# Kernel optimization log

Hardware: AMD Instinct MI355X
Metric: run time of the kernel (lower is better)

## Reference

```python
import jax, jax.numpy as jnp
import numpy as np

SHAPES = [(100, 168), (50, 84), (25, 42)]  # per-level (h, w)
HEADS, LEVELS, POINTS, EMBED = 8, 3, 8, 256
D_ANCHORS = 4  # num_Z_anchors; POINTS % D_ANCHORS == 0


def _bilinear_sample(v_l, loc, h, w):
    # v_l: [B, H, h*w, d]; loc: [B, nq, H, P, 2] normalized sampling locations
    B, nq, H, P, _ = loc.shape
    d = v_l.shape[-1]
    # F.grid_sample(align_corners=False, padding_mode='zeros'): pixel = loc*size - 0.5
    x = loc[..., 0] * w - 0.5
    y = loc[..., 1] * h - 0.5
    x0 = jnp.floor(x)
    y0 = jnp.floor(y)
    lx = x - x0
    ly = y - y0
    x0 = x0.astype(jnp.int32)
    y0 = y0.astype(jnp.int32)

    def gather(xi, yi):
        valid = ((xi >= 0) & (xi < w) & (yi >= 0) & (yi < h)).astype(v_l.dtype)
        idx = jnp.clip(yi, 0, h - 1) * w + jnp.clip(xi, 0, w - 1)  # [B,nq,H,P]
        idx = jnp.transpose(idx, (0, 2, 1, 3)).reshape(B, H, nq * P)
        vals = jnp.take_along_axis(v_l, idx[..., None], axis=2)  # [B,H,nq*P,d]
        vals = jnp.transpose(vals.reshape(B, H, nq, P, d), (0, 2, 1, 3, 4))
        return vals * valid[..., None]

    v00 = gather(x0, y0)
    v10 = gather(x0 + 1, y0)
    v01 = gather(x0, y0 + 1)
    v11 = gather(x0 + 1, y0 + 1)
    wx, wy = lx[..., None], ly[..., None]
    return (v00 * (1 - wx) * (1 - wy) + v10 * wx * (1 - wy)
            + v01 * (1 - wx) * wy + v11 * wx * wy)


def _msda(q, v, ref, Wv, bv, Ws, b_off, Wa, ba):
    # MSDeformableAttention3D: q [B,nq,C], v [B,nv,C], ref [B,nq,D,2]
    B, nq, C = q.shape
    nv = v.shape[1]
    d = C // HEADS
    val = (v @ Wv + bv).reshape(B, nv, HEADS, d).transpose(0, 2, 1, 3)  # [B,H,nv,d]
    off = (q @ Ws + b_off).reshape(B, nq, HEADS, LEVELS, POINTS, 2)
    aw = jax.nn.softmax((q @ Wa + ba).reshape(B, nq, HEADS, LEVELS * POINTS), axis=-1)
    aw = aw.reshape(B, nq, HEADS, LEVELS, POINTS)
    norm = jnp.array([[w, h] for (h, w) in SHAPES], dtype=q.dtype)  # offset_normalizer (w,h)
    off = off / norm[None, None, None, :, None, :]
    off = off.reshape(B, nq, HEADS, LEVELS, POINTS // D_ANCHORS, D_ANCHORS, 2)
    loc = ref[:, :, None, None, None, :, :] + off  # sampling_locations
    loc = loc.reshape(B, nq, HEADS, LEVELS, POINTS, 2)
    out = jnp.zeros((B, nq, HEADS, d), q.dtype)
    start = 0
    for lvl, (h, w) in enumerate(SHAPES):
        v_l = val[:, :, start:start + h * w, :]
        start += h * w
        s = _bilinear_sample(v_l, loc[:, :, :, lvl], h, w)  # [B,nq,H,P,d]
        out = out + jnp.einsum('bqhpd,bqhp->bqhd', s, aw[:, :, :, lvl])
    return out.reshape(B, nq, C)


def _forward(query, key, value, query_pos, reference_points_cam, bev_mask,
             Wv, bv, Ws, b_off, Wa, ba, Wo, bo):
    bs, nq, C = query.shape
    ncam = key.shape[0]
    inp_residual = query
    q = query + query_pos
    # key/value: [num_cams, l, bs, C] -> [bs*num_cams, l, C]
    v = jnp.transpose(value, (2, 0, 1, 3)).reshape(bs * ncam, -1, C)
    # dense equivalent of the per-camera query rebatching: run MSDA on all
    # queries per camera, then mask out non-hit queries (identical math)
    qc = jnp.broadcast_to(q[:, None], (bs, ncam, nq, C)).reshape(bs * ncam, nq, C)
    ref = jnp.transpose(reference_points_cam, (1, 0, 2, 3, 4)).reshape(bs * ncam, nq, D_ANCHORS, 2)
    out = _msda(qc, v, ref, Wv, bv, Ws, b_off, Wa, ba).reshape(bs, ncam, nq, C)
    hit = jnp.transpose(bev_mask.sum(-1) > 0, (1, 0, 2)).astype(out.dtype)  # [bs,ncam,nq]
    slots = (out * hit[..., None]).sum(axis=1)
    count = jnp.clip(hit.sum(axis=1), 1.0, None)
    slots = slots / count[..., None]
    slots = slots @ Wo + bo
    return slots + inp_residual  # dropout is identity at inference


def setup_inputs() -> dict:
    key0 = jax.random.key(0)
    ks = jax.random.split(key0, 12)
    bs, ncam, nq = 1, 6, 4096
    nv = sum(h * w for h, w in SHAPES)
    f = jnp.float32
    s = 0.02
    inp = {}
    inp['query'] = jax.random.normal(ks[0], (bs, nq, EMBED), f)
    inp['key'] = jax.random.normal(ks[1], (ncam, nv, bs, EMBED), f)
    inp['value'] = jax.random.normal(ks[2], (ncam, nv, bs, EMBED), f)
    inp['query_pos'] = jax.random.normal(ks[3], (bs, nq, EMBED), f)
    inp['reference_points_cam'] = jax.random.uniform(ks[4], (ncam, bs, nq, D_ANCHORS, 2), f)
    inp['bev_mask'] = jax.random.bernoulli(ks[5], 0.9, (ncam, bs, nq, D_ANCHORS))
    inp['spatial_shapes'] = jnp.array(SHAPES, dtype=jnp.int32)
    inp['level_start_index'] = jnp.array(np.cumsum([0] + [h * w for h, w in SHAPES[:-1]]), dtype=jnp.int32)
    inp['Wv'] = jax.random.normal(ks[6], (EMBED, EMBED), f) * s
    inp['bv'] = jnp.zeros((EMBED,), f)
    inp['Ws'] = jax.random.normal(ks[7], (EMBED, HEADS * LEVELS * POINTS * 2), f) * s
    inp['b_off'] = jax.random.normal(ks[8], (HEADS * LEVELS * POINTS * 2,), f) * 0.5
    inp['Wa'] = jax.random.normal(ks[9], (EMBED, HEADS * LEVELS * POINTS), f) * s
    inp['ba'] = jnp.zeros((HEADS * LEVELS * POINTS,), f)
    inp['Wo'] = jax.random.normal(ks[10], (EMBED, EMBED), f) * s
    inp['bo'] = jnp.zeros((EMBED,), f)
    return inp


def reference(query, key, value, query_pos, reference_points_cam, bev_mask,
              spatial_shapes, level_start_index,
              Wv, bv, Ws, b_off, Wa, ba, Wo, bo):
    return _forward(query, key, value, query_pos, reference_points_cam, bev_mask,
                    Wv, bv, Ws, b_off, Wa, ba, Wo, bo)
```

## Files before the change

kernel.cpp:

```cpp
#include <hip/hip_runtime.h>
#include <stdint.h>

#define NQ 4096
#define NCAM 6
#define NV 22050
#define M_TOTAL (NCAM * NV)

typedef __bf16 bf16x8 __attribute__((ext_vector_type(8)));
typedef float f32x4 __attribute__((ext_vector_type(4)));
typedef unsigned int u32x4 __attribute__((ext_vector_type(4)));

__device__ __forceinline__ unsigned short f2bf(float f) {
    union { float f; uint32_t u; } v; v.f = f;
    uint32_t u = v.u;
    uint32_t r = (u + 0x7FFFu + ((u >> 16) & 1u)) >> 16;
    return (unsigned short)r;
}
__device__ __forceinline__ float bf_lo(uint32_t u) {
    union { uint32_t u; float f; } v; v.u = u << 16; return v.f;
}
__device__ __forceinline__ float bf_hi(uint32_t u) {
    union { uint32_t u; float f; } v; v.u = u & 0xFFFF0000u; return v.f;
}
__device__ __forceinline__ int imin(int a, int b) { return a < b ? a : b; }
__device__ __forceinline__ int imax(int a, int b) { return a > b ? a : b; }

__global__ void wvt_kernel(const float* __restrict__ Wv, unsigned short* __restrict__ WvT) {
    int n = blockIdx.x, k = threadIdx.x;
    WvT[n * 256 + k] = f2bf(Wv[k * 256 + n]);
}

__global__ __launch_bounds__(256) void val_gemm(const float* __restrict__ A,
                                                const unsigned short* __restrict__ BT,
                                                const float* __restrict__ bv,
                                                unsigned short* __restrict__ C) {
    __shared__ unsigned char alds[2 * 4096];
    __shared__ unsigned char clds[64 * 528];
    const int t = threadIdx.x;
    const int w = t >> 6, lane = t & 63;
    const int r = lane & 15, g = lane >> 4;
    const int m_base = blockIdx.x * 64;

    const int srow = t >> 2, sc = t & 3;
    const float* asrc = A + (size_t)imin(m_base + srow, M_TOTAL - 1) * 256 + sc * 8;
    unsigned char* awr = &alds[sc * 1024 + srow * 16];

    f32x4 acc[4][4];
#pragma unroll
    for (int i = 0; i < 4; ++i)
#pragma unroll
        for (int j = 0; j < 4; ++j) acc[i][j] = (f32x4)0.0f;

    const unsigned short* brow[4];
#pragma unroll
    for (int ni = 0; ni < 4; ++ni)
        brow[ni] = BT + (size_t)(w * 64 + ni * 16 + r) * 256 + g * 8;

    {
        float4 lo = *reinterpret_cast<const float4*>(asrc);
        float4 hi = *reinterpret_cast<const float4*>(asrc + 4);
        bf16x8 av;
        av[0] = (__bf16)lo.x; av[1] = (__bf16)lo.y;
        av[2] = (__bf16)lo.z; av[3] = (__bf16)lo.w;
        av[4] = (__bf16)hi.x; av[5] = (__bf16)hi.y;
        av[6] = (__bf16)hi.z; av[7] = (__bf16)hi.w;
        *reinterpret_cast<u32x4*>(awr) = __builtin_bit_cast(u32x4, av);
    }
    __syncthreads();

#pragma unroll
    for (int ks = 0; ks < 8; ++ks) {
        float4 nlo, nhi;
        if (ks < 7) {
            nlo = *reinterpret_cast<const float4*>(asrc + (ks + 1) * 32);
            nhi = *reinterpret_cast<const float4*>(asrc + (ks + 1) * 32 + 4);
        }
        bf16x8 bfrag[4];
#pragma unroll
        for (int ni = 0; ni < 4; ++ni)
            bfrag[ni] = __builtin_bit_cast(bf16x8,
                *reinterpret_cast<const u32x4*>(brow[ni] + ks * 32));
        const unsigned char* abase = &alds[(ks & 1) * 4096 + g * 1024];
        bf16x8 afrag[4];
#pragma unroll
        for (int mi = 0; mi < 4; ++mi)
            afrag[mi] = __builtin_bit_cast(bf16x8,
                *reinterpret_cast<const u32x4*>(abase + (mi * 16 + r) * 16));
#pragma unroll
        for (int mi = 0; mi < 4; ++mi)
#pragma unroll
            for (int ni = 0; ni < 4; ++ni)
                acc[mi][ni] = __builtin_amdgcn_mfma_f32_16x16x32_bf16(
                    bfrag[ni], afrag[mi], acc[mi][ni], 0, 0, 0);
        if (ks < 7) {
            bf16x8 av;
            av[0] = (__bf16)nlo.x; av[1] = (__bf16)nlo.y;
            av[2] = (__bf16)nlo.z; av[3] = (__bf16)nlo.w;
            av[4] = (__bf16)nhi.x; av[5] = (__bf16)nhi.y;
            av[6] = (__bf16)nhi.z; av[7] = (__bf16)nhi.w;
            *reinterpret_cast<u32x4*>(awr + ((ks + 1) & 1) * 4096) =
                __builtin_bit_cast(u32x4, av);
            __syncthreads();
        }
    }

#pragma unroll
    for (int mi = 0; mi < 4; ++mi)
#pragma unroll
        for (int ni = 0; ni < 4; ++ni) {
            const int n0 = w * 64 + ni * 16 + g * 4;
            const float4 bb = *reinterpret_cast<const float4*>(bv + n0);
            uint2 pk;
            pk.x = (uint32_t)f2bf(acc[mi][ni][0] + bb.x) |
                   ((uint32_t)f2bf(acc[mi][ni][1] + bb.y) << 16);
            pk.y = (uint32_t)f2bf(acc[mi][ni][2] + bb.z) |
                   ((uint32_t)f2bf(acc[mi][ni][3] + bb.w) << 16);
            *reinterpret_cast<uint2*>(&clds[(mi * 16 + r) * 528 + n0 * 2]) = pk;
        }
    __syncthreads();

    const int mrow = t >> 2, part = t & 3;
    const int m = m_base + mrow;
    if (m < M_TOTAL) {
        unsigned int um = (unsigned int)m;
        unsigned int c = um / 22050u;
        unsigned int pix = um - c * 22050u;
        const unsigned char* src = &clds[mrow * 528 + part * 16];
#pragma unroll
        for (int hp = 0; hp < 8; ++hp) {
            u32x4 v = *reinterpret_cast<const u32x4*>(src + hp * 64);
            *reinterpret_cast<u32x4*>(
                C + (((size_t)c * 8 + hp) * NV + pix) * 32 + part * 8) = v;
        }
    }
}

__global__ __launch_bounds__(256) void proj_kernel(const float* __restrict__ query,
                                                   const float* __restrict__ qpos,
                                                   const float* __restrict__ Ws,
                                                   const float* __restrict__ b_off,
                                                   const float* __restrict__ Wa,
                                                   const float* __restrict__ ba,
                                                   float* __restrict__ off_ws,
                                                   float* __restrict__ aw_ws) {
    __shared__ float qrow[4][256];
    __shared__ float logits[4][192];
    const int t = threadIdx.x;
    const int qb = blockIdx.x * 4;
#pragma unroll
    for (int j = 0; j < 4; ++j)
        qrow[j][t] = query[(size_t)(qb + j) * 256 + t] + qpos[(size_t)(qb + j) * 256 + t];
    __syncthreads();

    const float invn[3][2] = {{1.f / 168.f, 1.f / 100.f},
                              {1.f / 84.f, 1.f / 50.f},
                              {1.f / 42.f, 1.f / 25.f}};
#pragma unroll
    for (int pass = 0; pass < 3; ++pass) {
        int u = t + pass * 256;
        if (u < 384) {
            float a0 = 0.f, a1 = 0.f, a2 = 0.f, a3 = 0.f;
            for (int k = 0; k < 256; ++k) {
                float w = Ws[k * 384 + u];
                a0 += qrow[0][k] * w; a1 += qrow[1][k] * w;
                a2 += qrow[2][k] * w; a3 += qrow[3][k] * w;
            }
            int lp = u >> 1;
            int l = (lp >> 3) % 3;
            float inv = invn[l][u & 1];
            float b = b_off[u];
            off_ws[(size_t)(qb + 0) * 384 + u] = (a0 + b) * inv;
            off_ws[(size_t)(qb + 1) * 384 + u] = (a1 + b) * inv;
            off_ws[(size_t)(qb + 2) * 384 + u] = (a2 + b) * inv;
            off_ws[(size_t)(qb + 3) * 384 + u] = (a3 + b) * inv;
        } else if (u < 576) {
            int u2 = u - 384;
            float a0 = 0.f, a1 = 0.f, a2 = 0.f, a3 = 0.f;
            for (int k = 0; k < 256; ++k) {
                float w = Wa[k * 192 + u2];
                a0 += qrow[0][k] * w; a1 += qrow[1][k] * w;
                a2 += qrow[2][k] * w; a3 += qrow[3][k] * w;
            }
            float b = ba[u2];
            logits[0][u2] = a0 + b; logits[1][u2] = a1 + b;
            logits[2][u2] = a2 + b; logits[3][u2] = a3 + b;
        }
    }
    __syncthreads();
    if (t < 32) {
        int jq = t >> 3, h = t & 7;
        float mx = -1e30f;
#pragma unroll
        for (int i = 0; i < 24; ++i) mx = fmaxf(mx, logits[jq][h * 24 + i]);
        float e[24];
        float s = 0.f;
#pragma unroll
        for (int i = 0; i < 24; ++i) { e[i] = __expf(logits[jq][h * 24 + i] - mx); s += e[i]; }
        float inv = 1.0f / s;
#pragma unroll
        for (int i = 0; i < 24; ++i)
            aw_ws[((size_t)(qb + jq) * 8 + h) * 24 + i] = e[i] * inv;
    }
}

__global__ __launch_bounds__(256) void sample_kernel(const unsigned short* __restrict__ val,
                                                     const float* __restrict__ rpc,
                                                     const float* __restrict__ off_ws,
                                                     const float* __restrict__ aw_ws,
                                                     unsigned short* __restrict__ out_cam) {
    const int t = threadIdx.x;
    const int qs = t >> 2;
    const int sub = t & 3;
    const int p = blockIdx.x;
    const int x = p & 7;
    const int g = x + 8 * (p >> 9);
    const int wblk = (p >> 3) & 63;
    const int c = g >> 3, h = g & 7;
    const int q = wblk * 64 + qs;
    const int pair = c * NQ + q;

    float refx[4], refy[4];
    const float* rp = rpc + (size_t)pair * 8;
#pragma unroll
    for (int a = 0; a < 4; ++a) { refx[a] = rp[2 * a]; refy[a] = rp[2 * a + 1]; }

    const unsigned short* vbase = val + (size_t)g * NV * 32 + sub * 8;
    const float* offp = off_ws + (size_t)q * 384 + h * 48;
    const float* awp = aw_ws + ((size_t)q * 8 + h) * 24;

    float acc[8];
#pragma unroll
    for (int i = 0; i < 8; ++i) acc[i] = 0.f;

    const int lw[3] = {168, 84, 42};
    const int lhh[3] = {100, 50, 25};
    const int lst[3] = {0, 16800, 21000};

#pragma unroll
    for (int l = 0; l < 3; ++l) {
        const int w = lw[l], hh = lhh[l];
        const float wf = (float)w, hf = (float)hh;
        const unsigned short* vlev = vbase + (size_t)lst[l] * 32;
#pragma unroll
        for (int pt = 0; pt < 8; ++pt) {
            const int a = pt & 3;
            float ox = offp[(l * 8 + pt) * 2 + 0];
            float oy = offp[(l * 8 + pt) * 2 + 1];
            float xx = fmaf(refx[a] + ox, wf, -0.5f);
            float yy = fmaf(refy[a] + oy, hf, -0.5f);
            float xf = floorf(xx), yf = floorf(yy);
            float lx = xx - xf, ly = yy - yf;
            int x0 = (int)xf, y0 = (int)yf;
            float aww = awp[l * 8 + pt];

            float wx0 = (x0 >= 0 && x0 < w) ? (1.f - lx) : 0.f;
            float wx1 = (x0 >= -1 && x0 < w - 1) ? lx : 0.f;
            float wy0 = ((y0 >= 0 && y0 < hh) ? (1.f - ly) : 0.f) * aww;
            float wy1 = ((y0 >= -1 && y0 < hh - 1) ? ly : 0.f) * aww;

            int x0c = imin(imax(x0, 0), w - 1);
            int x1c = imin(imax(x0 + 1, 0), w - 1);
            int y0c = imin(imax(y0, 0), hh - 1);
            int y1c = imin(imax(y0 + 1, 0), hh - 1);

            int r0 = y0c * w, r1 = y1c * w;
            u32x4 u00 = *reinterpret_cast<const u32x4*>(vlev + (size_t)(r0 + x0c) * 32);
            u32x4 u10 = *reinterpret_cast<const u32x4*>(vlev + (size_t)(r0 + x1c) * 32);
            u32x4 u01 = *reinterpret_cast<const u32x4*>(vlev + (size_t)(r1 + x0c) * 32);
            u32x4 u11 = *reinterpret_cast<const u32x4*>(vlev + (size_t)(r1 + x1c) * 32);

            float w00 = wx0 * wy0, w10 = wx1 * wy0, w01 = wx0 * wy1, w11 = wx1 * wy1;
#pragma unroll
            for (int i = 0; i < 4; ++i) {
                acc[2 * i] += w00 * bf_lo(u00[i]) + w10 * bf_lo(u10[i]) +
                              w01 * bf_lo(u01[i]) + w11 * bf_lo(u11[i]);
                acc[2 * i + 1] += w00 * bf_hi(u00[i]) + w10 * bf_hi(u10[i]) +
                                  w01 * bf_hi(u01[i]) + w11 * bf_hi(u11[i]);
            }
        }
    }

    u32x4 o;
#pragma unroll
    for (int i = 0; i < 4; ++i)
        o[i] = (uint32_t)f2bf(acc[2 * i]) | ((uint32_t)f2bf(acc[2 * i + 1]) << 16);
    *reinterpret_cast<u32x4*>(out_cam + (size_t)pair * 256 + h * 32 + sub * 8) = o;
}

__global__ __launch_bounds__(256) void combine_kernel(const unsigned short* __restrict__ out_cam,
                                                      const unsigned char* __restrict__ bev_mask,
                                                      const float* __restrict__ Wo,
                                                      const float* __restrict__ bo,
                                                      const float* __restrict__ query,
                                                      float* __restrict__ out) {
    __shared__ float s_lds[8][256];
    __shared__ unsigned int hitm[8];
    __shared__ float invc[8];
    const int t = threadIdx.x;
    const int qb = blockIdx.x * 8;

    if (t < 8) {
        int q = qb + t;
        unsigned int m = 0;
        int cnt = 0;
        for (int c = 0; c < 6; ++c) {
            const unsigned char* bm = bev_mask + ((size_t)c * NQ + q) * 4;
            if (bm[0] | bm[1] | bm[2] | bm[3]) { m |= (1u << c); cnt++; }
        }
        hitm[t] = m;
        invc[t] = 1.0f / (float)imax(cnt, 1);
    }
    __syncthreads();
#pragma unroll
    for (int j = 0; j < 8; ++j) {
        unsigned int m = hitm[j];
        float ic = invc[j];
        float s = 0.f;
#pragma unroll
        for (int c = 0; c < 6; ++c)
            if ((m >> c) & 1u) {
                unsigned short u = out_cam[((size_t)c * NQ + qb + j) * 256 + t];
                union { uint32_t u; float f; } v; v.u = ((uint32_t)u) << 16;
                s += v.f;
            }
        s_lds[j][t] = s * ic;
    }
    __syncthreads();
    float acc[8] = {0.f, 0.f, 0.f, 0.f, 0.f, 0.f, 0.f, 0.f};
    for (int k = 0; k < 256; ++k) {
        float wv = Wo[k * 256 + t];
#pragma unroll
        for (int j = 0; j < 8; ++j) acc[j] += s_lds[j][k] * wv;
    }
    float bb = bo[t];
#pragma unroll
    for (int j = 0; j < 8; ++j)
        out[(size_t)(qb + j) * 256 + t] = acc[j] + bb + query[(size_t)(qb + j) * 256 + t];
}

extern "C" void kernel_launch(void* const* d_in, const int* in_sizes, int n_in,
                              void* d_out, int out_size, void* d_ws, size_t ws_size,
                              hipStream_t stream) {
    const float* query = (const float*)d_in[0];
    const float* value = (const float*)d_in[2];
    const float* qpos = (const float*)d_in[3];
    const float* rpc = (const float*)d_in[4];
    const unsigned char* bev = (const unsigned char*)d_in[5];
    const float* Wv = (const float*)d_in[8];
    const float* bv = (const float*)d_in[9];
    const float* Ws = (const float*)d_in[10];
    const float* b_off = (const float*)d_in[11];
    const float* Wa = (const float*)d_in[12];
    const float* ba = (const float*)d_in[13];
    const float* Wo = (const float*)d_in[14];
    const float* bo = (const float*)d_in[15];
    float* out = (float*)d_out;

    char* ws = (char*)d_ws;
    unsigned short* val_ws = (unsigned short*)ws;
    size_t o = 67737600;
    float* off_ws = (float*)(ws + o);            o += 6291456;
    float* aw_ws = (float*)(ws + o);             o += 3145728;
    unsigned short* out_cam = (unsigned short*)(ws + o); o += 12582912;
    unsigned short* WvT = (unsigned short*)(ws + o);

    wvt_kernel<<<256, 256, 0, stream>>>(Wv, WvT);
    proj_kernel<<<NQ / 4, 256, 0, stream>>>(query, qpos, Ws, b_off, Wa, ba, off_ws, aw_ws);
    val_gemm<<<(M_TOTAL + 63) / 64, 256, 0, stream>>>(value, WvT, bv, val_ws);
    sample_kernel<<<3072, 256, 0, stream>>>(val_ws, rpc, off_ws, aw_ws, out_cam);
    combine_kernel<<<NQ / 8, 256, 0, stream>>>(out_cam, bev, Wo, bo, query, out);
}
```

Before: 212.6 us.

## Split sampling-coordinate computation across sub-lanes and share via LDS

Before, each of the four threads serving one query/head pair recomputed the same 24 bilinear offsets and weights. Now each thread computes 6 of the 24 points and writes the corner indices and combined weights to shared memory. After a block barrier, all four threads read them back to do the gathers. This removes the 4x redundant address and weight arithmetic and the redundant offset/weight loads, at the cost of about 50KB of LDS per block (which may limit occupancy), a __syncthreads, and LDS traffic.

```diff
diff --git a/kernel.cpp b/kernel.cpp
--- a/kernel.cpp
+++ b/kernel.cpp
@@ -208,6 +208,7 @@
                                                      const float* __restrict__ off_ws,
                                                      const float* __restrict__ aw_ws,
                                                      unsigned short* __restrict__ out_cam) {
+    __shared__ u32x4 dlds[64 * 49];
     const int t = threadIdx.x;
     const int qs = t >> 2;
     const int sub = t & 3;
@@ -219,39 +220,34 @@
     const int q = wblk * 64 + qs;
     const int pair = c * NQ + q;
 
-    float refx[4], refy[4];
-    const float* rp = rpc + (size_t)pair * 8;
-#pragma unroll
-    for (int a = 0; a < 4; ++a) { refx[a] = rp[2 * a]; refy[a] = rp[2 * a + 1]; }
-
-    const unsigned short* vbase = val + (size_t)g * NV * 32 + sub * 8;
-    const float* offp = off_ws + (size_t)q * 384 + h * 48;
-    const float* awp = aw_ws + ((size_t)q * 8 + h) * 24;
-
-    float acc[8];
-#pragma unroll
-    for (int i = 0; i < 8; ++i) acc[i] = 0.f;
-
-    const int lw[3] = {168, 84, 42};
-    const int lhh[3] = {100, 50, 25};
-    const int lst[3] = {0, 16800, 21000};
-
-#pragma unroll
-    for (int l = 0; l < 3; ++l) {
-        const int w = lw[l], hh = lhh[l];
-        const float wf = (float)w, hf = (float)hh;
-        const unsigned short* vlev = vbase + (size_t)lst[l] * 32;
-#pragma unroll
-        for (int pt = 0; pt < 8; ++pt) {
+    {
+        const float* rp = rpc + (size_t)pair * 8;
+        float4 r01 = *reinterpret_cast<const float4*>(rp);
+        float4 r23 = *reinterpret_cast<const float4*>(rp + 4);
+        const float* offp = off_ws + (size_t)q * 384 + h * 48;
+        const float* awp = aw_ws + ((size_t)q * 8 + h) * 24;
+#pragma unroll
+        for (int i = 0; i < 6; ++i) {
+            const int pt = sub * 6 + i;
+            const int lvl = pt >> 3;
+            const int w = 168 >> lvl, hh = 100 >> lvl;
+            const int lst = (lvl == 0) ? 0 : ((lvl == 1) ? 16800 : 21000);
             const int a = pt & 3;
-            float ox = offp[(l * 8 + pt) * 2 + 0];
-            float oy = offp[(l * 8 + pt) * 2 + 1];
-            float xx = fmaf(refx[a] + ox, wf, -0.5f);
-            float yy = fmaf(refy[a] + oy, hf, -0.5f);
+            float rx01 = (a & 1) ? r01.z : r01.x;
+            float ry01 = (a & 1) ? r01.w : r01.y;
+            float rx23 = (a & 1) ? r23.z : r23.x;
+            float ry23 = (a & 1) ? r23.w : r23.y;
+            float rx = (a & 2) ? rx23 : rx01;
+            float ry = (a & 2) ? ry23 : ry01;
+
+            float ox = offp[pt * 2 + 0];
+            float oy = offp[pt * 2 + 1];
+            float aww = awp[pt];
+            float xx = fmaf(rx + ox, (float)w, -0.5f);
+            float yy = fmaf(ry + oy, (float)hh, -0.5f);
             float xf = floorf(xx), yf = floorf(yy);
             float lx = xx - xf, ly = yy - yf;
             int x0 = (int)xf, y0 = (int)yf;
-            float aww = awp[l * 8 + pt];
 
             float wx0 = (x0 >= 0 && x0 < w) ? (1.f - lx) : 0.f;
             float wx1 = (x0 >= -1 && x0 < w - 1) ? lx : 0.f;
@@ -262,21 +258,42 @@
             int x1c = imin(imax(x0 + 1, 0), w - 1);
             int y0c = imin(imax(y0, 0), hh - 1);
             int y1c = imin(imax(y0 + 1, 0), hh - 1);
-
-            int r0 = y0c * w, r1 = y1c * w;
-            u32x4 u00 = *reinterpret_cast<const u32x4*>(vlev + (size_t)(r0 + x0c) * 32);
-            u32x4 u10 = *reinterpret_cast<const u32x4*>(vlev + (size_t)(r0 + x1c) * 32);
-            u32x4 u01 = *reinterpret_cast<const u32x4*>(vlev + (size_t)(r1 + x0c) * 32);
-            u32x4 u11 = *reinterpret_cast<const u32x4*>(vlev + (size_t)(r1 + x1c) * 32);
-
-            float w00 = wx0 * wy0, w10 = wx1 * wy0, w01 = wx0 * wy1, w11 = wx1 * wy1;
-#pragma unroll
-            for (int i = 0; i < 4; ++i) {
-                acc[2 * i] += w00 * bf_lo(u00[i]) + w10 * bf_lo(u10[i]) +
-                              w01 * bf_lo(u01[i]) + w11 * bf_lo(u11[i]);
-                acc[2 * i + 1] += w00 * bf_hi(u00[i]) + w10 * bf_hi(u10[i]) +
-                                  w01 * bf_hi(u01[i]) + w11 * bf_hi(u11[i]);
-            }
+            int r0 = lst + y0c * w, r1 = lst + y1c * w;
+
+            u32x4 doff;
+            doff[0] = (unsigned)(r0 + x0c);
+            doff[1] = (unsigned)(r0 + x1c);
+            doff[2] = (unsigned)(r1 + x0c);
+            doff[3] = (unsigned)(r1 + x1c);
+            f32x4 dw;
+            dw[0] = wx0 * wy0; dw[1] = wx1 * wy0;
+            dw[2] = wx0 * wy1; dw[3] = wx1 * wy1;
+            dlds[qs * 49 + pt * 2 + 0] = doff;
+            dlds[qs * 49 + pt * 2 + 1] = __builtin_bit_cast(u32x4, dw);
+        }
+    }
+    __syncthreads();
+
+    const unsigned short* vg = val + (size_t)g * NV * 32 + sub * 8;
+    float acc[8];
+#pragma unroll
+    for (int i = 0; i < 8; ++i) acc[i] = 0.f;
+
+#pragma unroll
+    for (int pt = 0; pt < 24; ++pt) {
+        u32x4 doff = dlds[qs * 49 + pt * 2 + 0];
+        f32x4 dw = __builtin_bit_cast(f32x4, dlds[qs * 49 + pt * 2 + 1]);
+        u32x4 u00 = *reinterpret_cast<const u32x4*>(vg + (size_t)doff[0] * 32);
+        u32x4 u10 = *reinterpret_cast<const u32x4*>(vg + (size_t)doff[1] * 32);
+        u32x4 u01 = *reinterpret_cast<const u32x4*>(vg + (size_t)doff[2] * 32);
+        u32x4 u11 = *reinterpret_cast<const u32x4*>(vg + (size_t)doff[3] * 32);
+        float w00 = dw[0], w10 = dw[1], w01 = dw[2], w11 = dw[3];
+#pragma unroll
+        for (int i = 0; i < 4; ++i) {
+            acc[2 * i] += w00 * bf_lo(u00[i]) + w10 * bf_lo(u10[i]) +
+                          w01 * bf_lo(u01[i]) + w11 * bf_lo(u11[i]);
+            acc[2 * i + 1] += w00 * bf_hi(u00[i]) + w10 * bf_hi(u10[i]) +
+                              w01 * bf_hi(u01[i]) + w11 * bf_hi(u11[i]);
         }
     }
 
```

After: 202.0 us. -5.0%, faster.
